# Performance work log

Hardware: AMD Instinct MI355X
Metric: run time of the kernel (lower is better)

Reference implementation:

```python
import jax, jax.numpy as jnp
import numpy as np

B, POOL, PACK = 4096, 45, 15
E, D, V = 512, 8, 30000  # embedding_dim, internal_dims, num_cards
SQRT_D = float(np.sqrt(D))


def setup_inputs() -> dict:
    key = jax.random.key(0)
    ks = jax.random.split(key, 12)
    s = 0.02
    return {
        "pool": jax.random.randint(ks[0], (B, POOL), 0, V),
        "pack": jax.random.randint(ks[1], (B, PACK), 0, V),
        "wins": jax.random.uniform(ks[2], (B,), dtype=jnp.float32),
        "ranks": jax.random.uniform(ks[3], (B,), dtype=jnp.float32),
        "emb_table": jax.random.normal(ks[4], (V, E), dtype=jnp.float32) * s,
        "win_w": jax.random.normal(ks[5], (E, 1), dtype=jnp.float32) * s,
        "win_b": jnp.zeros((E,), dtype=jnp.float32),
        "rank_w": jax.random.normal(ks[6], (E, 1), dtype=jnp.float32) * s,
        "rank_b": jnp.zeros((E,), dtype=jnp.float32),
        "q_w": jax.random.normal(ks[7], (D, E), dtype=jnp.float32) * s,
        "k_w": jax.random.normal(ks[8], (D, E), dtype=jnp.float32) * s,
        "v_w": jax.random.normal(ks[9], (D, E), dtype=jnp.float32) * s,
        "sc_w": jax.random.normal(ks[10], (1, D), dtype=jnp.float32) * s,
        "sc_b": jnp.zeros((1,), dtype=jnp.float32),
    }


def reference(pool, pack, wins, ranks, emb_table, win_w, win_b,
              rank_w, rank_b, q_w, k_w, v_w, sc_w, sc_b):
    pool_emb = emb_table[pool]                                   # [B, POOL, E]
    pack_emb = emb_table[pack]                                   # [B, PACK, E]
    win_emb = wins[:, None, None] * win_w[:, 0] + win_b          # [B, 1, E]
    rank_emb = ranks[:, None, None] * rank_w[:, 0] + rank_b      # [B, 1, E]
    pool_full = jnp.concatenate([pool_emb, win_emb, rank_emb], axis=1)  # [B, POOL+2, E]
    pool_full = jax.nn.relu(pool_full)
    q = jnp.einsum("bke,de->bkd", pack_emb, q_w)                 # [B, PACK, D]
    k = jnp.einsum("bpe,de->bpd", pool_full, k_w)                # [B, POOL+2, D]
    v = jnp.einsum("bpe,de->bpd", pool_full, v_w)                # [B, POOL+2, D]
    scores = jnp.einsum("bkd,bpd->bkp", q, k) / SQRT_D
    attn = jax.nn.softmax(jax.nn.relu(scores), axis=-1)          # [B, PACK, POOL+2]
    context = jnp.einsum("bkp,bpd->bkd", attn, v)                # [B, PACK, D]
    context = jax.nn.leaky_relu(context, negative_slope=0.01)
    logits = jnp.einsum("bkd,od->bko", context, sc_w) + sc_b     # [B, PACK, 1]
    return logits[..., 0]                                        # [B, PACK]
```

## Files before the change

kernel.cpp:

```cpp
#include <hip/hip_runtime.h>

#define B_N 4096
#define POOL_N 45
#define PACK_N 15
#define E_N 512
#define D_N 8
#define V_N 30000

#define WT_SZ  (E_N * 24)
#define TAB_SZ (V_N * 24)

__global__ __launch_bounds__(256) void k_transpose_w(const float* __restrict__ q_w,
                                                     const float* __restrict__ k_w,
                                                     const float* __restrict__ v_w,
                                                     float* __restrict__ wt) {
  int i = blockIdx.x * 256 + threadIdx.x;
  if (i >= E_N * 24) return;
  int e = i / 24, j = i % 24;
  float val = (j < 8) ? q_w[j * E_N + e]
            : (j < 16) ? k_w[(j - 8) * E_N + e]
                       : v_w[(j - 16) * E_N + e];
  wt[i] = val;
}

__global__ __launch_bounds__(1024, 8) void k_build_tab(const float* __restrict__ emb,
                                                       const float* __restrict__ wt,
                                                       float* __restrict__ tab) {
  __shared__ float red[8][64][25];
  int lane = threadIdx.x & 63;
  int w = __builtin_amdgcn_readfirstlane(threadIdx.x >> 6);
  int r = blockIdx.x * 64 + lane;
  float acc[24];
#pragma unroll
  for (int j = 0; j < 24; ++j) acc[j] = 0.f;
  if (r < V_N) {
    const float* a = emb + (size_t)r * E_N + w * 32;
    const float* wp = wt + (w * 32) * 24;
#pragma unroll 2
    for (int i = 0; i < 8; ++i) {
      float4 av = ((const float4*)a)[i];
      float xs[4] = {av.x, av.y, av.z, av.w};
#pragma unroll
      for (int c = 0; c < 4; ++c) {
        float x = xs[c];
        float xr = fmaxf(x, 0.f);
        const float* wr = wp + (i * 4 + c) * 24;
#pragma unroll
        for (int j = 0; j < 8; ++j) acc[j] = fmaf(x, wr[j], acc[j]);
#pragma unroll
        for (int j = 8; j < 24; ++j) acc[j] = fmaf(xr, wr[j], acc[j]);
      }
    }
  }
  if (w < 8) {
#pragma unroll
    for (int j = 0; j < 24; ++j) red[w][lane][j] = acc[j];
  }
  __syncthreads();
  if (w >= 8) {
#pragma unroll
    for (int j = 0; j < 24; ++j) red[w - 8][lane][j] += acc[j];
  }
  __syncthreads();
  for (int o = threadIdx.x; o < 1536; o += 1024) {
    int row = o / 24, col = o - row * 24;
    int r_out = blockIdx.x * 64 + row;
    if (r_out < V_N) {
      float v = 0.f;
#pragma unroll
      for (int s = 0; s < 8; ++s) v += red[s][row][col];
      tab[(size_t)r_out * 24 + col] = v;
    }
  }
}

__global__ __launch_bounds__(256) void k_build_aux(const float* __restrict__ wins,
                                                   const float* __restrict__ ranks,
                                                   const float* __restrict__ win_w,
                                                   const float* __restrict__ win_b,
                                                   const float* __restrict__ rank_w,
                                                   const float* __restrict__ rank_b,
                                                   const float* __restrict__ wt,
                                                   float* __restrict__ aux) {
  __shared__ float red[16][16][17];
  int t = threadIdx.x;
  int bl = t & 15, seg = t >> 4;
  int which = blockIdx.y;
  int b = blockIdx.x * 16 + bl;
  float s = which ? ranks[b] : wins[b];
  const float* ww = which ? rank_w : win_w;
  const float* wb = which ? rank_b : win_b;
  float acc[16];
#pragma unroll
  for (int j = 0; j < 16; ++j) acc[j] = 0.f;
  int e0 = seg * 32;
#pragma unroll 4
  for (int e = e0; e < e0 + 32; ++e) {
    float x = fmaf(s, ww[e], wb[e]);
    float xr = fmaxf(x, 0.f);
    const float* wr = wt + e * 24 + 8;
#pragma unroll
    for (int j = 0; j < 16; ++j) acc[j] = fmaf(xr, wr[j], acc[j]);
  }
#pragma unroll
  for (int j = 0; j < 16; ++j) red[seg][bl][j] = acc[j];
  __syncthreads();
  int bi = t >> 4, j = t & 15;
  float v = 0.f;
#pragma unroll
  for (int sg = 0; sg < 16; ++sg) v += red[sg][bi][j];
  aux[(size_t)(blockIdx.x * 16 + bi) * 32 + which * 16 + j] = v;
}

__global__ __launch_bounds__(256) void k_main(const int* __restrict__ pool,
                                              const int* __restrict__ pack,
                                              const float* __restrict__ tab,
                                              const float* __restrict__ aux,
                                              const float* __restrict__ sc_w,
                                              const float* __restrict__ sc_b,
                                              float* __restrict__ out) {
  int grp = threadIdx.x >> 5;
  int lane = threadIdx.x & 31;
  int b = blockIdx.x * 8 + grp;
  int i0 = pool[(size_t)b * POOL_N + lane];
  int i1 = (lane < POOL_N - 32) ? pool[(size_t)b * POOL_N + 32 + lane] : 0;
  int k = (lane < PACK_N) ? lane : 0;
  int qidx = pack[(size_t)b * PACK_N + k];
  const float* qr = tab + (size_t)qidx * 24;
  float4 qa = *(const float4*)qr;
  float4 qb = *(const float4*)(qr + 4);
  const float rs = 0.35355339059327373f;
  const float* auxb = aux + (size_t)b * 32;

  float m = 0.f, sum = 0.f;
  float ctx[8] = {0.f, 0.f, 0.f, 0.f, 0.f, 0.f, 0.f, 0.f};

  auto att_step = [&](const float* kr) {
    float4 k0 = *(const float4*)kr;
    float4 k1 = *(const float4*)(kr + 4);
    float4 v0 = *(const float4*)(kr + 8);
    float4 v1 = *(const float4*)(kr + 12);
    float d = qa.x * k0.x;
    d = fmaf(qa.y, k0.y, d);
    d = fmaf(qa.z, k0.z, d);
    d = fmaf(qa.w, k0.w, d);
    d = fmaf(qb.x, k1.x, d);
    d = fmaf(qb.y, k1.y, d);
    d = fmaf(qb.z, k1.z, d);
    d = fmaf(qb.w, k1.w, d);
    d = fmaxf(d * rs, 0.f);
    float t = __expf(-fabsf(d - m));
    bool up = d > m;
    float sc = up ? t : 1.f;
    float e = up ? 1.f : t;
    m = fmaxf(m, d);
    sum = fmaf(sum, sc, e);
    ctx[0] = fmaf(ctx[0], sc, e * v0.x);
    ctx[1] = fmaf(ctx[1], sc, e * v0.y);
    ctx[2] = fmaf(ctx[2], sc, e * v0.z);
    ctx[3] = fmaf(ctx[3], sc, e * v0.w);
    ctx[4] = fmaf(ctx[4], sc, e * v1.x);
    ctx[5] = fmaf(ctx[5], sc, e * v1.y);
    ctx[6] = fmaf(ctx[6], sc, e * v1.z);
    ctx[7] = fmaf(ctx[7], sc, e * v1.w);
  };

#pragma unroll 8
  for (int p = 0; p < 32; ++p) {
    int pi = __shfl(i0, p, 32);
    att_step(tab + (size_t)pi * 24 + 8);
  }
#pragma unroll
  for (int p = 0; p < 13; ++p) {
    int pi = __shfl(i1, p, 32);
    att_step(tab + (size_t)pi * 24 + 8);
  }
  att_step(auxb);
  att_step(auxb + 16);

  float inv = 1.f / sum;
  float logit = 0.f;
#pragma unroll
  for (int d0 = 0; d0 < 8; ++d0) {
    float c = ctx[d0] * inv;
    c = (c > 0.f) ? c : 0.01f * c;
    logit = fmaf(c, sc_w[d0], logit);
  }
  logit += sc_b[0];
  if (lane < PACK_N) out[(size_t)b * PACK_N + lane] = logit;
}

extern "C" void kernel_launch(void* const* d_in, const int* in_sizes, int n_in,
                              void* d_out, int out_size, void* d_ws, size_t ws_size,
                              hipStream_t stream) {
  const int* pool = (const int*)d_in[0];
  const int* pack = (const int*)d_in[1];
  const float* wins = (const float*)d_in[2];
  const float* ranks = (const float*)d_in[3];
  const float* emb = (const float*)d_in[4];
  const float* win_w = (const float*)d_in[5];
  const float* win_b = (const float*)d_in[6];
  const float* rank_w = (const float*)d_in[7];
  const float* rank_b = (const float*)d_in[8];
  const float* q_w = (const float*)d_in[9];
  const float* k_w = (const float*)d_in[10];
  const float* v_w = (const float*)d_in[11];
  const float* sc_w = (const float*)d_in[12];
  const float* sc_b = (const float*)d_in[13];

  float* ws = (float*)d_ws;
  float* wt = ws;
  float* tab = ws + WT_SZ;
  float* aux = ws + WT_SZ + TAB_SZ;
  float* out = (float*)d_out;

  hipLaunchKernelGGL(k_transpose_w, dim3(48), dim3(256), 0, stream,
                     q_w, k_w, v_w, wt);
  hipLaunchKernelGGL(k_build_tab, dim3((V_N + 63) / 64), dim3(1024), 0, stream,
                     emb, wt, tab);
  hipLaunchKernelGGL(k_build_aux, dim3(B_N / 16, 2), dim3(256), 0, stream,
                     wins, ranks, win_w, win_b, rank_w, rank_b, wt, aux);
  hipLaunchKernelGGL(k_main, dim3(B_N / 8), dim3(256), 0, stream,
                     pool, pack, tab, aux, sc_w, sc_b, out);
}
```

Before: 63.35 us.

## Split table build over E halves with partial buffers and a reduce kernel

The projection-table build now splits the 512-wide embedding dimension into two halves on a second grid axis. Each half runs 512-thread blocks and writes a partial 24-column table to a new workspace region, and a new kernel then sums the two partials into the final table. The goal is more, smaller blocks for better occupancy and latency hiding on the memory-bound gather of the 61 MB embedding table. The cost is an extra launch plus a write and reread of two partial tables, and the inner loop is now fully unrolled.

```diff
diff --git a/kernel.cpp b/kernel.cpp
--- a/kernel.cpp
+++ b/kernel.cpp
@@ -9,6 +9,7 @@
 
 #define WT_SZ  (E_N * 24)
 #define TAB_SZ (V_N * 24)
+#define AUX_SZ (B_N * 32)
 
 __global__ __launch_bounds__(256) void k_transpose_w(const float* __restrict__ q_w,
                                                      const float* __restrict__ k_w,
@@ -23,20 +24,21 @@
   wt[i] = val;
 }
 
-__global__ __launch_bounds__(1024, 8) void k_build_tab(const float* __restrict__ emb,
-                                                       const float* __restrict__ wt,
-                                                       float* __restrict__ tab) {
+__global__ __launch_bounds__(512) void k_build_tab(const float* __restrict__ emb,
+                                                   const float* __restrict__ wt,
+                                                   float* __restrict__ part) {
   __shared__ float red[8][64][25];
   int lane = threadIdx.x & 63;
   int w = __builtin_amdgcn_readfirstlane(threadIdx.x >> 6);
+  int half = blockIdx.y;
   int r = blockIdx.x * 64 + lane;
   float acc[24];
 #pragma unroll
   for (int j = 0; j < 24; ++j) acc[j] = 0.f;
   if (r < V_N) {
-    const float* a = emb + (size_t)r * E_N + w * 32;
-    const float* wp = wt + (w * 32) * 24;
-#pragma unroll 2
+    const float* a = emb + (size_t)r * E_N + half * 256 + w * 32;
+    const float* wp = wt + (half * 256 + w * 32) * 24;
+#pragma unroll
     for (int i = 0; i < 8; ++i) {
       float4 av = ((const float4*)a)[i];
       float xs[4] = {av.x, av.y, av.z, av.w};
@@ -52,25 +54,30 @@
       }
     }
   }
-  if (w < 8) {
-#pragma unroll
-    for (int j = 0; j < 24; ++j) red[w][lane][j] = acc[j];
-  }
+#pragma unroll
+  for (int j = 0; j < 24; ++j) red[w][lane][j] = acc[j];
   __syncthreads();
-  if (w >= 8) {
-#pragma unroll
-    for (int j = 0; j < 24; ++j) red[w - 8][lane][j] += acc[j];
-  }
-  __syncthreads();
-  for (int o = threadIdx.x; o < 1536; o += 1024) {
+  float* po = part + (size_t)half * TAB_SZ;
+  for (int o = threadIdx.x; o < 1536; o += 512) {
     int row = o / 24, col = o - row * 24;
     int r_out = blockIdx.x * 64 + row;
     if (r_out < V_N) {
       float v = 0.f;
 #pragma unroll
       for (int s = 0; s < 8; ++s) v += red[s][row][col];
-      tab[(size_t)r_out * 24 + col] = v;
+      po[(size_t)r_out * 24 + col] = v;
     }
+  }
+}
+
+__global__ __launch_bounds__(256) void k_reduce_tab(const float* __restrict__ part,
+                                                    float* __restrict__ tab) {
+  int i = blockIdx.x * 256 + threadIdx.x;
+  if (i < TAB_SZ / 4) {
+    float4 a = ((const float4*)part)[i];
+    float4 b = ((const float4*)(part + TAB_SZ))[i];
+    float4 o = {a.x + b.x, a.y + b.y, a.z + b.z, a.w + b.w};
+    ((float4*)tab)[i] = o;
   }
 }
 
@@ -212,12 +219,15 @@
   float* wt = ws;
   float* tab = ws + WT_SZ;
   float* aux = ws + WT_SZ + TAB_SZ;
+  float* part = ws + WT_SZ + TAB_SZ + AUX_SZ;
   float* out = (float*)d_out;
 
   hipLaunchKernelGGL(k_transpose_w, dim3(48), dim3(256), 0, stream,
                      q_w, k_w, v_w, wt);
-  hipLaunchKernelGGL(k_build_tab, dim3((V_N + 63) / 64), dim3(1024), 0, stream,
-                     emb, wt, tab);
+  hipLaunchKernelGGL(k_build_tab, dim3((V_N + 63) / 64, 2), dim3(512), 0, stream,
+                     emb, wt, part);
+  hipLaunchKernelGGL(k_reduce_tab, dim3((TAB_SZ / 4 + 255) / 256), dim3(256), 0, stream,
+                     part, tab);
   hipLaunchKernelGGL(k_build_aux, dim3(B_N / 16, 2), dim3(256), 0, stream,
                      wins, ranks, win_w, win_b, rank_w, rank_b, wt, aux);
   hipLaunchKernelGGL(k_main, dim3(B_N / 8), dim3(256), 0, stream,
```

Result: slower. 82.92 us (+30.9%).
